# Optimization experiments

Measured on AMD Instinct MI355X. Metric: run time of the kernel, lower is better.

Reference implementation:

```python
import jax, jax.numpy as jnp
import numpy as np

N_NODES = 50000
N_EDGES = 800000
IN_CH, HID_CH, OUT_CH = 512, 128, 64


def gcn_conv(x, W, b, src, dst, num_nodes):
    """PyG GCNConv: add self-loops, sym-normalize, linear, scatter-add, bias.
    x: [N, Fin], W: [Fout, Fin], b: [Fout], src/dst: [E] int."""
    loop = jnp.arange(num_nodes, dtype=src.dtype)
    src2 = jnp.concatenate([src, loop])  # [E+N]
    dst2 = jnp.concatenate([dst, loop])
    deg = jax.ops.segment_sum(jnp.ones_like(dst2, dtype=x.dtype), dst2,
                              num_segments=num_nodes)  # in-degree + 1
    d_inv_sqrt = jnp.where(deg > 0, jax.lax.rsqrt(deg), 0.0)
    norm = d_inv_sqrt[src2] * d_inv_sqrt[dst2]  # [E+N]
    h = x @ W.T  # [N, Fout]
    msg = h[src2] * norm[:, None]  # [E+N, Fout] -- dominant memory traffic
    out = jax.ops.segment_sum(msg, dst2, num_segments=num_nodes)
    return out + b


def setup_inputs() -> dict:
    key = jax.random.key(0)
    ks = jax.random.split(key, 8)
    x = jax.random.normal(ks[0], (N_NODES, IN_CH), dtype=jnp.float32)
    edge_index = jax.random.randint(ks[1], (2, N_EDGES), 0, N_NODES, dtype=jnp.int64)
    s1 = 1.0 / np.sqrt(IN_CH)
    s2 = 1.0 / np.sqrt(HID_CH)
    W1 = jax.random.normal(ks[2], (HID_CH, IN_CH), dtype=jnp.float32) * s1
    b1 = jnp.zeros((HID_CH,), dtype=jnp.float32)
    W_mu = jax.random.normal(ks[3], (OUT_CH, HID_CH), dtype=jnp.float32) * s2
    b_mu = jnp.zeros((OUT_CH,), dtype=jnp.float32)
    W_logstd = jax.random.normal(ks[4], (OUT_CH, HID_CH), dtype=jnp.float32) * s2
    b_logstd = jnp.zeros((OUT_CH,), dtype=jnp.float32)
    return {"x": x, "edge_index": edge_index, "W1": W1, "b1": b1,
            "W_mu": W_mu, "b_mu": b_mu, "W_logstd": W_logstd, "b_logstd": b_logstd}


def reference(x, edge_index, W1, b1, W_mu, b_mu, W_logstd, b_logstd):
    src, dst = edge_index[0], edge_index[1]
    n = x.shape[0]
    h = jax.nn.relu(gcn_conv(x, W1, b1, src, dst, n))
    mu = gcn_conv(h, W_mu, b_mu, src, dst, n)
    logstd = gcn_conv(h, W_logstd, b_logstd, src, dst, n)
    return (mu, logstd)
```

## Files before the change

### kernel.cpp

```cpp
#include <hip/hip_runtime.h>

constexpr int FIN = 512;
constexpr int FH  = 128;
constexpr int FO  = 64;

typedef short short8 __attribute__((ext_vector_type(8)));
typedef float f32x4 __attribute__((ext_vector_type(4)));

__device__ __forceinline__ unsigned short f2bf(float f) {
    unsigned u = __float_as_uint(f);
    u += 0x7fffu + ((u >> 16) & 1u);
    return (unsigned short)(u >> 16);
}
__device__ __forceinline__ float bf2f(unsigned short h) {
    return __uint_as_float((unsigned)h << 16);
}
__device__ __forceinline__ float bflo(unsigned v) { return __uint_as_float(v << 16); }
__device__ __forceinline__ float bfhi(unsigned v) { return __uint_as_float(v & 0xffff0000u); }


__global__ void pre_kernel(const int* __restrict__ dst, int* __restrict__ cnt, int E,
                           const float* __restrict__ W1, unsigned short* __restrict__ W1b,
                           const float* __restrict__ Wmu, const float* __restrict__ Wlg,
                           unsigned short* __restrict__ Wh, unsigned short* __restrict__ Wl,
                           int cntB) {
    int b = blockIdx.x;
    if (b < cntB) {
        int i = b * 256 + threadIdx.x;
        if (i < E) atomicAdd(&cnt[dst[i]], 1);
    } else if (b < cntB + 64) {
        int i = (b - cntB) * 256 + threadIdx.x;
        float4 v = ((const float4*)W1)[i];
        ushort4 p;
        p.x = f2bf(v.x); p.y = f2bf(v.y); p.z = f2bf(v.z); p.w = f2bf(v.w);
        ((ushort4*)W1b)[i] = p;
    } else {
        int i = (b - cntB - 64) * 256 + threadIdx.x;
        int r = i >> 7, c = i & 127;
        float f = (r < 64) ? Wmu[r * 128 + c] : Wlg[(r - 64) * 128 + c];
        unsigned short h = f2bf(f);
        Wh[i] = h;
        Wl[i] = f2bf(f - bf2f(h));
    }
}


__global__ void scan1_kernel(const int* __restrict__ cnt, int* __restrict__ offs,
                             int* __restrict__ bsum, float* __restrict__ dinv, int n) {
    __shared__ int sdata[256];
    int t = threadIdx.x;
    int base = blockIdx.x * 1024 + t * 4;
    int4 c = make_int4(0, 0, 0, 0);
    if (base + 3 < n) {
        c = *(const int4*)(cnt + base);
    } else {
        if (base + 0 < n) c.x = cnt[base + 0];
        if (base + 1 < n) c.y = cnt[base + 1];
        if (base + 2 < n) c.z = cnt[base + 2];
        if (base + 3 < n) c.w = cnt[base + 3];
    }
    if (base + 0 < n) dinv[base + 0] = rsqrtf((float)(c.x + 1));
    if (base + 1 < n) dinv[base + 1] = rsqrtf((float)(c.y + 1));
    if (base + 2 < n) dinv[base + 2] = rsqrtf((float)(c.z + 1));
    if (base + 3 < n) dinv[base + 3] = rsqrtf((float)(c.w + 1));

    int s0 = c.x + c.y + c.z + c.w;
    sdata[t] = s0;
    __syncthreads();
    for (int off = 1; off < 256; off <<= 1) {
        int v = (t >= off) ? sdata[t - off] : 0;
        __syncthreads();
        sdata[t] += v;
        __syncthreads();
    }
    int excl = sdata[t] - s0;
    if (t == 255) bsum[blockIdx.x] = sdata[255];
    if (base + 0 < n) offs[base + 0] = excl;
    if (base + 1 < n) offs[base + 1] = excl + c.x;
    if (base + 2 < n) offs[base + 2] = excl + c.x + c.y;
    if (base + 3 < n) offs[base + 3] = excl + c.x + c.y + c.z;
}

__global__ void scan2_kernel(int* __restrict__ bsum, int nb) {
    __shared__ int sdata[256];
    int t = threadIdx.x;
    int v = (t < nb) ? bsum[t] : 0;
    sdata[t] = v;
    __syncthreads();
    for (int off = 1; off < 256; off <<= 1) {
        int u = (t >= off) ? sdata[t - off] : 0;
        __syncthreads();
        sdata[t] += u;
        __syncthreads();
    }
    if (t < nb) bsum[t] = sdata[t] - v;
}

__global__ void scan3_kernel(int* __restrict__ offs, const int* __restrict__ bsum,
                             int n, int E) {
    int i = blockIdx.x * blockDim.x + threadIdx.x;
    if (i < n) offs[i] += bsum[i >> 10];
    if (i == 0) offs[n] = E;
}


__global__ void fill_kernel(const int* __restrict__ src, const int* __restrict__ dst,
                            const float* __restrict__ dinv, const int* __restrict__ offs,
                            int* __restrict__ cursor, int2* __restrict__ esort, int E) {
    int i = blockIdx.x * blockDim.x + threadIdx.x;
    if (i < E) {
        int s = src[i];
        int d = dst[i];
        int pos = offs[d] + atomicAdd(&cursor[d], 1);
        float w = dinv[s] * dinv[d];
        esort[pos] = make_int2(s, __float_as_int(w));
    }
}


__global__ void spmm_kernel(const unsigned int* __restrict__ hin, const int* __restrict__ offs,
                            const int2* __restrict__ esort, const float* __restrict__ dinv,
                            const float* __restrict__ bias, unsigned int* __restrict__ hout,
                            int n, int relu) {
    int gid = blockIdx.x * blockDim.x + threadIdx.x;
    int node = gid >> 6;
    int lane = threadIdx.x & 63;
    if (node >= n) return;
    float di = dinv[node];
    unsigned hv = hin[(size_t)node * 64 + lane];
    float ax = di * di * bflo(hv);
    float ay = di * di * bfhi(hv);
    int p = offs[node];
    int end = offs[node + 1];
    if ((p & 1) && p < end) {
        int2 e = esort[p];
        unsigned v = hin[(size_t)e.x * 64 + lane];
        float w = __int_as_float(e.y);
        ax = fmaf(w, bflo(v), ax); ay = fmaf(w, bfhi(v), ay);
        ++p;
    }
    for (; p + 8 <= end; p += 8) {
        int4 q0 = *(const int4*)(esort + p + 0);
        int4 q1 = *(const int4*)(esort + p + 2);
        int4 q2 = *(const int4*)(esort + p + 4);
        int4 q3 = *(const int4*)(esort + p + 6);
        unsigned v0 = hin[(size_t)q0.x * 64 + lane];
        unsigned v1 = hin[(size_t)q0.z * 64 + lane];
        unsigned v2 = hin[(size_t)q1.x * 64 + lane];
        unsigned v3 = hin[(size_t)q1.z * 64 + lane];
        unsigned v4 = hin[(size_t)q2.x * 64 + lane];
        unsigned v5 = hin[(size_t)q2.z * 64 + lane];
        unsigned v6 = hin[(size_t)q3.x * 64 + lane];
        unsigned v7 = hin[(size_t)q3.z * 64 + lane];
        float w0 = __int_as_float(q0.y), w1 = __int_as_float(q0.w);
        float w2 = __int_as_float(q1.y), w3 = __int_as_float(q1.w);
        float w4 = __int_as_float(q2.y), w5 = __int_as_float(q2.w);
        float w6 = __int_as_float(q3.y), w7 = __int_as_float(q3.w);
        ax = fmaf(w0, bflo(v0), ax); ay = fmaf(w0, bfhi(v0), ay);
        ax = fmaf(w1, bflo(v1), ax); ay = fmaf(w1, bfhi(v1), ay);
        ax = fmaf(w2, bflo(v2), ax); ay = fmaf(w2, bfhi(v2), ay);
        ax = fmaf(w3, bflo(v3), ax); ay = fmaf(w3, bfhi(v3), ay);
        ax = fmaf(w4, bflo(v4), ax); ay = fmaf(w4, bfhi(v4), ay);
        ax = fmaf(w5, bflo(v5), ax); ay = fmaf(w5, bfhi(v5), ay);
        ax = fmaf(w6, bflo(v6), ax); ay = fmaf(w6, bfhi(v6), ay);
        ax = fmaf(w7, bflo(v7), ax); ay = fmaf(w7, bfhi(v7), ay);
    }
    for (; p + 2 <= end; p += 2) {
        int4 q = *(const int4*)(esort + p);
        unsigned v0 = hin[(size_t)q.x * 64 + lane];
        unsigned v1 = hin[(size_t)q.z * 64 + lane];
        float w0 = __int_as_float(q.y), w1 = __int_as_float(q.w);
        ax = fmaf(w0, bflo(v0), ax); ay = fmaf(w0, bfhi(v0), ay);
        ax = fmaf(w1, bflo(v1), ax); ay = fmaf(w1, bfhi(v1), ay);
    }
    if (p < end) {
        int2 e = esort[p];
        unsigned v = hin[(size_t)e.x * 64 + lane];
        float w = __int_as_float(e.y);
        ax = fmaf(w, bflo(v), ax); ay = fmaf(w, bfhi(v), ay);
    }
    if (bias) {
        float2 b = ((const float2*)bias)[lane];
        ax += b.x; ay += b.y;
    }
    if (relu) { ax = fmaxf(ax, 0.f); ay = fmaxf(ay, 0.f); }
    unsigned o = (unsigned)f2bf(ax) | ((unsigned)f2bf(ay) << 16);
    hout[(size_t)node * 64 + lane] = o;
}


__global__ __launch_bounds__(1024, 4) void gemm1_kernel(
    const float* __restrict__ X, const unsigned short* __restrict__ Wb,
    unsigned short* __restrict__ out, int M, int nstrips) {
    extern __shared__ __align__(16) unsigned short Bs[];
    int tid = threadIdx.x;

    #pragma unroll
    for (int j = 0; j < 8; ++j) {
        int f = tid + j * 1024;
        int row = f >> 6;
        unsigned addr = ((unsigned)f << 4) ^ ((unsigned)(row & 7) << 4);
        *(short8*)((char*)Bs + addr) = ((const short8*)Wb)[f];
    }
    __syncthreads();

    int lane = tid & 63, wid = tid >> 6;
    int fr = lane & 15, fq = lane >> 4;
    int s = blockIdx.x * 16 + wid;
    if (s >= nstrips) return;
    int row0 = s * 16;
    int arow = row0 + fr; if (arow >= M) arow = M - 1;
    const float* ap = X + (size_t)arow * FIN + fq * 8;

    f32x4 acc[8] = {};

    float4 c0 = *(const float4*)(ap + 0);
    float4 c1 = *(const float4*)(ap + 4);
    float4 c2 = *(const float4*)(ap + 32);
    float4 c3 = *(const float4*)(ap + 36);

    #pragma unroll
    for (int kk = 0; kk < 8; ++kk) {
        int k0 = kk * 64;
        float4 d0 = c0, d1 = c1, d2 = c2, d3 = c3;
        if (kk < 7) {
            c0 = *(const float4*)(ap + k0 + 64);
            c1 = *(const float4*)(ap + k0 + 68);
            c2 = *(const float4*)(ap + k0 + 96);
            c3 = *(const float4*)(ap + k0 + 100);
        }
        short8 af0, af1;
        af0[0] = (short)f2bf(d0.x); af0[1] = (short)f2bf(d0.y);
        af0[2] = (short)f2bf(d0.z); af0[3] = (short)f2bf(d0.w);
        af0[4] = (short)f2bf(d1.x); af0[5] = (short)f2bf(d1.y);
        af0[6] = (short)f2bf(d1.z); af0[7] = (short)f2bf(d1.w);
        af1[0] = (short)f2bf(d2.x); af1[1] = (short)f2bf(d2.y);
        af1[2] = (short)f2bf(d2.z); af1[3] = (short)f2bf(d2.w);
        af1[4] = (short)f2bf(d3.x); af1[5] = (short)f2bf(d3.y);
        af1[6] = (short)f2bf(d3.z); af1[7] = (short)f2bf(d3.w);

        int cb0 = k0 * 2 + fq * 16;
        #pragma unroll
        for (int c = 0; c < 8; ++c) {
            int br = c * 16 + fr;
            short8 b0 = *(const short8*)((const char*)Bs + br * 1024 +
                                         ((unsigned)cb0 ^ ((unsigned)(br & 7) << 4)));
            acc[c] = __builtin_amdgcn_mfma_f32_16x16x32_bf16(af0, b0, acc[c], 0, 0, 0);
        }
        int cb1 = cb0 + 64;
        #pragma unroll
        for (int c = 0; c < 8; ++c) {
            int br = c * 16 + fr;
            short8 b1 = *(const short8*)((const char*)Bs + br * 1024 +
                                         ((unsigned)cb1 ^ ((unsigned)(br & 7) << 4)));
            acc[c] = __builtin_amdgcn_mfma_f32_16x16x32_bf16(af1, b1, acc[c], 0, 0, 0);
        }
    }

    #pragma unroll
    for (int c = 0; c < 8; ++c) {
        #pragma unroll
        for (int j = 0; j < 4; ++j) {
            int row = row0 + fq * 4 + j;
            if (row < M) out[(size_t)row * FH + c * 16 + fr] = f2bf(acc[c][j]);
        }
    }
}


__global__ __launch_bounds__(512) void gemm2_kernel(
    const unsigned short* __restrict__ Xb,
    const unsigned short* __restrict__ Wh, const unsigned short* __restrict__ Wl,
    float* __restrict__ outA, float* __restrict__ outB,
    const float* __restrict__ biasA, const float* __restrict__ biasB,
    int M, int nstrips) {
    __shared__ __align__(16) unsigned short WhS[128 * 128];
    __shared__ __align__(16) unsigned short WlS[128 * 128];
    int tid = threadIdx.x;

    #pragma unroll
    for (int j = 0; j < 4; ++j) {
        int f = tid + j * 512;
        int row = f >> 4;
        unsigned addr = ((unsigned)f * 16u) ^ ((unsigned)(row & 7) << 4);
        *(short8*)((char*)WhS + addr) = ((const short8*)Wh)[f];
        *(short8*)((char*)WlS + addr) = ((const short8*)Wl)[f];
    }
    __syncthreads();

    int lane = tid & 63, wid = tid >> 6;
    int fr = lane & 15, fq = lane >> 4;
    int s = blockIdx.x * 8 + wid;
    if (s >= nstrips) return;
    int row0 = s * 16;
    int arow = row0 + fr; if (arow > M - 1) arow = M - 1;
    const unsigned short* ap = Xb + (size_t)arow * FH + fq * 8;

    short8 a0 = *(const short8*)(ap + 0);
    short8 a1 = *(const short8*)(ap + 32);
    short8 a2 = *(const short8*)(ap + 64);
    short8 a3 = *(const short8*)(ap + 96);

    f32x4 acc[8] = {};

    auto proc = [&](int k0, short8 a) {
        int cb = k0 * 2 + fq * 16;
        #pragma unroll
        for (int c = 0; c < 8; ++c) {
            int lr = c * 16 + fr;
            unsigned addr = ((unsigned)(lr * 256 + cb)) ^ ((unsigned)(lr & 7) << 4);
            short8 bh = *(const short8*)((const char*)WhS + addr);
            short8 bl = *(const short8*)((const char*)WlS + addr);
            acc[c] = __builtin_amdgcn_mfma_f32_16x16x32_bf16(a, bh, acc[c], 0, 0, 0);
            acc[c] = __builtin_amdgcn_mfma_f32_16x16x32_bf16(a, bl, acc[c], 0, 0, 0);
        }
    };
    proc(0, a0);
    proc(32, a1);
    proc(64, a2);
    proc(96, a3);

    #pragma unroll
    for (int c = 0; c < 8; ++c) {
        float* outp = (c < 4) ? outA : outB;
        const float* bp = (c < 4) ? biasA : biasB;
        int col = (c & 3) * 16 + fr;
        float bv = bp[col];
        #pragma unroll
        for (int j = 0; j < 4; ++j) {
            int row = row0 + fq * 4 + j;
            if (row < M) outp[(size_t)row * FO + col] = acc[c][j] + bv;
        }
    }
}


extern "C" void kernel_launch(void* const* d_in, const int* in_sizes, int n_in,
                              void* d_out, int out_size, void* d_ws, size_t ws_size,
                              hipStream_t stream) {
    const float* x   = (const float*)d_in[0];
    const int*   ei  = (const int*)d_in[1];
    const float* W1  = (const float*)d_in[2];
    const float* b1  = (const float*)d_in[3];
    const float* Wmu = (const float*)d_in[4];
    const float* bmu = (const float*)d_in[5];
    const float* Wlg = (const float*)d_in[6];
    const float* blg = (const float*)d_in[7];

    const int n = in_sizes[0] / FIN;
    const int E = in_sizes[1] / 2;
    const int* src = ei;
    const int* dst = ei + E;
    const int nstrips = (n + 15) / 16;

    char* ws = (char*)d_ws;
    size_t off = 0;
    auto alloc = [&](size_t bytes) -> void* {
        void* p = ws + off;
        off = (off + bytes + 255) & ~((size_t)255);
        return p;
    };
    int*   cnt    = (int*)  alloc((size_t)n * 4);
    int*   offs   = (int*)  alloc((size_t)(n + 1) * 4);
    int*   cursor = (int*)  alloc((size_t)n * 4);
    int*   bsum   = (int*)  alloc(1024);
    float* dinv   = (float*)alloc((size_t)n * 4);
    int2*  esort  = (int2*) alloc((size_t)E * 8);
    unsigned short* hbf  = (unsigned short*)alloc((size_t)n * FH * 2);
    unsigned short* h1bf = (unsigned short*)alloc((size_t)n * FH * 2);
    unsigned short* ah2b = (unsigned short*)alloc((size_t)n * FH * 2);
    unsigned short* W1b = (unsigned short*)alloc((size_t)FH * FIN * 2);
    unsigned short* W2h = (unsigned short*)alloc((size_t)FH * FH * 2);
    unsigned short* W2l = (unsigned short*)alloc((size_t)FH * FH * 2);

    hipMemsetAsync(cnt, 0, (size_t)n * 4, stream);
    hipMemsetAsync(cursor, 0, (size_t)n * 4, stream);

    int cntB = (E + 255) / 256;
    pre_kernel<<<cntB + 128, 256, 0, stream>>>(dst, cnt, E, W1, W1b, Wmu, Wlg, W2h, W2l, cntB);

    int nb = (n + 1023) / 1024;
    scan1_kernel<<<nb, 256, 0, stream>>>(cnt, offs, bsum, dinv, n);
    scan2_kernel<<<1, 256, 0, stream>>>(bsum, nb);
    scan3_kernel<<<(n + 255) / 256, 256, 0, stream>>>(offs, bsum, n, E);

    fill_kernel<<<(E + 255) / 256, 256, 0, stream>>>(src, dst, dinv, offs, cursor, esort, E);

    gemm1_kernel<<<(nstrips + 15) / 16, 1024, 128 * 1024, stream>>>(x, W1b, hbf, n, nstrips);
    spmm_kernel<<<(n + 3) / 4, 256, 0, stream>>>(
        (const unsigned*)hbf, offs, esort, dinv, b1, (unsigned*)h1bf, n, 1);
    spmm_kernel<<<(n + 3) / 4, 256, 0, stream>>>(
        (const unsigned*)h1bf, offs, esort, dinv, nullptr, (unsigned*)ah2b, n, 0);
    float* outmu = (float*)d_out;
    float* outlg = outmu + (size_t)n * FO;
    gemm2_kernel<<<512, 512, 0, stream>>>(ah2b, W2h, W2l, outmu, outlg, bmu, blg, n, nstrips);
}
```

Measured before the change: 197.7 us.

## Make gemm1 persistent with two-deep prefetch and resize gemm2 grid

gemm1 becomes a persistent kernel: a fixed grid of 256 blocks loops over row strips, so the 128 KB bf16 W1 copy is loaded into shared memory once per block rather than once per 16 strips. The X prefetch is deepened from one to two K-chunks ahead using alternating register buffers, to hide global load latency. gemm2's grid changes from a fixed 512 blocks to one block per 8 strips. This costs extra registers for the deeper prefetch, and the gemm2 change assumes its hidden loop handles a grid sized this way.

```diff
diff --git a/kernel.cpp b/kernel.cpp
--- a/kernel.cpp
+++ b/kernel.cpp
@@ -206,63 +206,77 @@
 
     int lane = tid & 63, wid = tid >> 6;
     int fr = lane & 15, fq = lane >> 4;
-    int s = blockIdx.x * 16 + wid;
-    if (s >= nstrips) return;
-    int row0 = s * 16;
-    int arow = row0 + fr; if (arow >= M) arow = M - 1;
-    const float* ap = X + (size_t)arow * FIN + fq * 8;
-
-    f32x4 acc[8] = {};
-
-    float4 c0 = *(const float4*)(ap + 0);
-    float4 c1 = *(const float4*)(ap + 4);
-    float4 c2 = *(const float4*)(ap + 32);
-    float4 c3 = *(const float4*)(ap + 36);
-
-    #pragma unroll
-    for (int kk = 0; kk < 8; ++kk) {
-        int k0 = kk * 64;
-        float4 d0 = c0, d1 = c1, d2 = c2, d3 = c3;
-        if (kk < 7) {
-            c0 = *(const float4*)(ap + k0 + 64);
-            c1 = *(const float4*)(ap + k0 + 68);
-            c2 = *(const float4*)(ap + k0 + 96);
-            c3 = *(const float4*)(ap + k0 + 100);
+
+    for (int s = wid * gridDim.x + blockIdx.x; s < nstrips; s += 16 * gridDim.x) {
+        int row0 = s * 16;
+        int arow = row0 + fr; if (arow >= M) arow = M - 1;
+        const float* ap = X + (size_t)arow * FIN + fq * 8;
+
+        f32x4 acc[8] = {};
+        float4 pa0[4], pa1[4];
+        pa0[0] = *(const float4*)(ap + 0);
+        pa0[1] = *(const float4*)(ap + 4);
+        pa0[2] = *(const float4*)(ap + 32);
+        pa0[3] = *(const float4*)(ap + 36);
+        pa1[0] = *(const float4*)(ap + 64);
+        pa1[1] = *(const float4*)(ap + 68);
+        pa1[2] = *(const float4*)(ap + 96);
+        pa1[3] = *(const float4*)(ap + 100);
+
+        #pragma unroll
+        for (int kk = 0; kk < 8; ++kk) {
+            int k0 = kk * 64;
+            float4 d0, d1, d2, d3;
+            if ((kk & 1) == 0) { d0 = pa0[0]; d1 = pa0[1]; d2 = pa0[2]; d3 = pa0[3]; }
+            else               { d0 = pa1[0]; d1 = pa1[1]; d2 = pa1[2]; d3 = pa1[3]; }
+            if (kk < 6) {
+                if ((kk & 1) == 0) {
+                    pa0[0] = *(const float4*)(ap + k0 + 128);
+                    pa0[1] = *(const float4*)(ap + k0 + 132);
+                    pa0[2] = *(const float4*)(ap + k0 + 160);
+                    pa0[3] = *(const float4*)(ap + k0 + 164);
+                } else {
+                    pa1[0] = *(const float4*)(ap + k0 + 128);
+                    pa1[1] = *(const float4*)(ap + k0 + 132);
+                    pa1[2] = *(const float4*)(ap + k0 + 160);
+                    pa1[3] = *(const float4*)(ap + k0 + 164);
+                }
+            }
+            short8 af0, af1;
+            af0[0] = (short)f2bf(d0.x); af0[1] = (short)f2bf(d0.y);
+            af0[2] = (short)f2bf(d0.z); af0[3] = (short)f2bf(d0.w);
+            af0[4] = (short)f2bf(d1.x); af0[5] = (short)f2bf(d1.y);
+            af0[6] = (short)f2bf(d1.z); af0[7] = (short)f2bf(d1.w);
+            af1[0] = (short)f2bf(d2.x); af1[1] = (short)f2bf(d2.y);
+            af1[2] = (short)f2bf(d2.z); af1[3] = (short)f2bf(d2.w);
+            af1[4] = (short)f2bf(d3.x); af1[5] = (short)f2bf(d3.y);
+            af1[6] = (short)f2bf(d3.z); af1[7] = (short)f2bf(d3.w);
+
+            int cb0 = k0 * 2 + fq * 16;
+            #pragma unroll
+            for (int c = 0; c < 8; ++c) {
+                int br = c * 16 + fr;
+                short8 b0 = *(const short8*)((const char*)Bs + br * 1024 +
+                                             ((unsigned)cb0 ^ ((unsigned)(br & 7) << 4)));
+                acc[c] = __builtin_amdgcn_mfma_f32_16x16x32_bf16(af0, b0, acc[c], 0, 0, 0);
+            }
+            int cb1 = cb0 + 64;
+            #pragma unroll
+            for (int c = 0; c < 8; ++c) {
+                int br = c * 16 + fr;
+                short8 b1 = *(const short8*)((const char*)Bs + br * 1024 +
+                                             ((unsigned)cb1 ^ ((unsigned)(br & 7) << 4)));
+                acc[c] = __builtin_amdgcn_mfma_f32_16x16x32_bf16(af1, b1, acc[c], 0, 0, 0);
+            }
         }
-        short8 af0, af1;
-        af0[0] = (short)f2bf(d0.x); af0[1] = (short)f2bf(d0.y);
-        af0[2] = (short)f2bf(d0.z); af0[3] = (short)f2bf(d0.w);
-        af0[4] = (short)f2bf(d1.x); af0[5] = (short)f2bf(d1.y);
-        af0[6] = (short)f2bf(d1.z); af0[7] = (short)f2bf(d1.w);
-        af1[0] = (short)f2bf(d2.x); af1[1] = (short)f2bf(d2.y);
-        af1[2] = (short)f2bf(d2.z); af1[3] = (short)f2bf(d2.w);
-        af1[4] = (short)f2bf(d3.x); af1[5] = (short)f2bf(d3.y);
-        af1[6] = (short)f2bf(d3.z); af1[7] = (short)f2bf(d3.w);
-
-        int cb0 = k0 * 2 + fq * 16;
+
         #pragma unroll
         for (int c = 0; c < 8; ++c) {
-            int br = c * 16 + fr;
-            short8 b0 = *(const short8*)((const char*)Bs + br * 1024 +
-                                         ((unsigned)cb0 ^ ((unsigned)(br & 7) << 4)));
-            acc[c] = __builtin_amdgcn_mfma_f32_16x16x32_bf16(af0, b0, acc[c], 0, 0, 0);
-        }
-        int cb1 = cb0 + 64;
-        #pragma unroll
-        for (int c = 0; c < 8; ++c) {
-            int br = c * 16 + fr;
-            short8 b1 = *(const short8*)((const char*)Bs + br * 1024 +
-                                         ((unsigned)cb1 ^ ((unsigned)(br & 7) << 4)));
-            acc[c] = __builtin_amdgcn_mfma_f32_16x16x32_bf16(af1, b1, acc[c], 0, 0, 0);
-        }
-    }
-
-    #pragma unroll
-    for (int c = 0; c < 8; ++c) {
-        #pragma unroll
-        for (int j = 0; j < 4; ++j) {
-            int row = row0 + fq * 4 + j;
-            if (row < M) out[(size_t)row * FH + c * 16 + fr] = f2bf(acc[c][j]);
+            #pragma unroll
+            for (int j = 0; j < 4; ++j) {
+                int row = row0 + fq * 4 + j;
+                if (row < M) out[(size_t)row * FH + c * 16 + fr] = f2bf(acc[c][j]);
+            }
         }
     }
 }
@@ -386,12 +400,13 @@
 
     fill_kernel<<<(E + 255) / 256, 256, 0, stream>>>(src, dst, dinv, offs, cursor, esort, E);
 
-    gemm1_kernel<<<(nstrips + 15) / 16, 1024, 128 * 1024, stream>>>(x, W1b, hbf, n, nstrips);
+    gemm1_kernel<<<256, 1024, 128 * 1024, stream>>>(x, W1b, hbf, n, nstrips);
     spmm_kernel<<<(n + 3) / 4, 256, 0, stream>>>(
         (const unsigned*)hbf, offs, esort, dinv, b1, (unsigned*)h1bf, n, 1);
     spmm_kernel<<<(n + 3) / 4, 256, 0, stream>>>(
         (const unsigned*)h1bf, offs, esort, dinv, nullptr, (unsigned*)ah2b, n, 0);
     float* outmu = (float*)d_out;
     float* outlg = outmu + (size_t)n * FO;
-    gemm2_kernel<<<512, 512, 0, stream>>>(ah2b, W2h, W2l, outmu, outlg, bmu, blg, n, nstrips);
-}
+    gemm2_kernel<<<(nstrips + 7) / 8, 512, 0, stream>>>(
+        ah2b, W2h, W2l, outmu, outlg, bmu, blg, n, nstrips);
+}
```

Measured after the change: 377.5 us. 1.91x slower.
